# Kernel tuning notes

Measured on AMD Instinct MI355X. Metric: run time of the kernel, lower is better.

## Reference

```python
import jax, jax.numpy as jnp
import numpy as np

NB_USERS = 100000
NB_MOVIES = 20000
K = 64
N = 2000000
MAX_RATING = 5.0


def setup_inputs() -> dict:
    key = jax.random.key(0)
    ks = jax.random.split(key, 8)
    return {
        "x_users": jnp.arange(NB_USERS, dtype=jnp.int32),  # every user queried once -> original's user filter is identity
        "x_movies": jax.random.randint(ks[0], (NB_USERS,), 0, NB_MOVIES),
        "data_users": jax.random.randint(ks[1], (N,), 0, NB_USERS),
        "data_movies": jax.random.randint(ks[2], (N,), 0, NB_MOVIES),
        "data_ratings": jax.random.uniform(ks[3], (N,), dtype=jnp.float32) * MAX_RATING,
        "movies_features": jax.random.normal(ks[4], (NB_MOVIES, K), dtype=jnp.float32),
        "W_r": jax.random.normal(ks[5], (K, 1), dtype=jnp.float32) * 0.1,
        "b_r": jnp.zeros((K,), dtype=jnp.float32),
        "W_c": jax.random.normal(ks[6], (K, K), dtype=jnp.float32) * 0.1,
        "b_c": jnp.zeros((K,), dtype=jnp.float32),
        "w_out": jax.random.normal(ks[7], (1, 1), dtype=jnp.float32),
        "b_out": jnp.zeros((1,), dtype=jnp.float32),
    }


def reference(x_users, x_movies, data_users, data_movies, data_ratings,
              movies_features, W_r, b_r, W_c, b_c, w_out, b_out):
    # movies_ratings_func: Linear(1,k) + sigmoid on normalized ratings
    ratings = jax.nn.sigmoid((data_ratings[:, None] / MAX_RATING) @ W_r.T + b_r)  # [N,k]
    # combined_func: Linear(k,k) + sigmoid on (gathered movie feats * rating emb)
    rbm = jax.nn.sigmoid((movies_features[data_movies] * ratings) @ W_c.T + b_c)  # [N,k]
    # scatter-add aggregate per user
    rating_by_user = jax.ops.segment_sum(rbm, data_users, num_segments=NB_USERS)  # [U,k]
    nb_ratings = jax.ops.segment_sum(jnp.ones((N,), dtype=rbm.dtype), data_users,
                                     num_segments=NB_USERS)  # [U]
    # ignore_if_seen=True path (faithful, including rbm indexed by movie id as in original)
    rating_by_user = rating_by_user.at[x_users].add(-rbm[x_movies])
    nb_ratings = nb_ratings.at[x_users].set(jnp.maximum(jnp.float32(1.0), nb_ratings[x_users] - 1.0))
    user_features = rating_by_user[x_users] / nb_ratings[x_users][:, None]  # [B,k]
    movie_features = movies_features[x_movies]  # [B,k]
    r = (movie_features * user_features).mean(-1, keepdims=True)  # [B,1]
    r = (r @ w_out.T + b_out) * MAX_RATING  # result_func then *max_rating
    return r.reshape(-1)
```

## Files before the change

kernel.cpp:

```cpp
#include <hip/hip_runtime.h>

#define NB_USERS 100000
#define NB_MOVIES 20000
#define KDIM 64
#define NPTS 2000000
#define NTILES (NPTS / 64)
#define RQ_LEVELS 8192
#define NBUCK 391
#define CHUNK 4096
#define NCHUNK ((NPTS + CHUNK - 1) / CHUNK)
#define BCAP 6400
#define LOG2E 1.44269504088896f

typedef _Float16 f16x8 __attribute__((ext_vector_type(8)));
typedef float    f32x4 __attribute__((ext_vector_type(4)));

__device__ __forceinline__ float sigmoidf(float z) {
    return 1.0f / (1.0f + __expf(-z));
}
__device__ __forceinline__ float sigmoid_w(float w) {
    return __builtin_amdgcn_rcpf(1.0f + __builtin_amdgcn_exp2f(w));
}


__global__ __launch_bounds__(256) void mf16_kernel(
    const float* __restrict__ mf, _Float16* __restrict__ mf16)
{
    const int idx = blockIdx.x * 256 + threadIdx.x;
    if (idx < NB_MOVIES * KDIM) mf16[idx] = (_Float16)mf[idx];
}

__global__ __launch_bounds__(256) void rtab16_kernel(
    const float* __restrict__ W_r, const float* __restrict__ b_r,
    _Float16* __restrict__ rtab16)
{
    const int idx = blockIdx.x * 256 + threadIdx.x;
    const int total = (RQ_LEVELS + 1) * KDIM;
    if (idx >= total) return;
    const int q = idx >> 6, k = idx & 63;
    rtab16[idx] = (_Float16)sigmoidf(fmaf((float)q * (1.0f / RQ_LEVELS), W_r[k], b_r[k]));
}

__global__ __launch_bounds__(256) void wcfrag_kernel(
    const float* __restrict__ W_c, _Float16* __restrict__ wcfrag)
{
    const int idx = blockIdx.x * 256 + threadIdx.x;
    if (idx >= 8 * 64) return;
    const int ntkt = idx >> 6;
    const int nt = ntkt >> 1, kt = ntkt & 1;
    const int lane = idx & 63;
    const float* src = &W_c[(nt * 16 + (lane & 15)) * KDIM + kt * 32 + (lane >> 4) * 8];
    _Float16* dst = wcfrag + (size_t)ntkt * 512 + lane * 8;
    #pragma unroll
    for (int e = 0; e < 8; ++e) dst[e] = (_Float16)(src[e] * -LOG2E);
}

__global__ __launch_bounds__(256) void bucket_hist_kernel(
    const int* __restrict__ du, int* __restrict__ bhist)
{
    __shared__ int h[NBUCK];
    for (int b = threadIdx.x; b < NBUCK; b += 256) h[b] = 0;
    __syncthreads();
    int i = blockIdx.x * 256 + threadIdx.x;
    const int stride = gridDim.x * 256;
    for (; i < NPTS; i += stride) atomicAdd(&h[du[i] >> 8], 1);
    __syncthreads();
    for (int b = threadIdx.x; b < NBUCK; b += 256)
        if (h[b]) atomicAdd(&bhist[b], h[b]);
}

__global__ __launch_bounds__(256) void bscan_kernel(
    const int* __restrict__ bhist, int* __restrict__ bstart, int* __restrict__ bcursor)
{
    __shared__ int s[512];
    const int t = threadIdx.x;
    const int v0 = (t < NBUCK) ? bhist[t] : 0;
    const int v1 = (t + 256 < NBUCK) ? bhist[t + 256] : 0;
    s[t] = v0; s[t + 256] = v1;
    __syncthreads();
    for (int d = 1; d < 512; d <<= 1) {
        const int a0 = (t >= d) ? s[t - d] : 0;
        const int a1 = (t + 256 >= d) ? s[t + 256 - d] : 0;
        __syncthreads();
        s[t] += a0; s[t + 256] += a1;
        __syncthreads();
    }
    if (t < NBUCK)       { bstart[t]       = s[t] - v0;       bcursor[t]       = s[t] - v0; }
    if (t + 256 < NBUCK) { bstart[t + 256] = s[t + 256] - v1; bcursor[t + 256] = s[t + 256] - v1; }
}

__global__ __launch_bounds__(256) void binA_kernel(
    const int* __restrict__ du, const int* __restrict__ dm,
    const float* __restrict__ dr,
    int* __restrict__ bcursor, uint2* __restrict__ binned)
{
    __shared__ uint2 buf[CHUNK];
    __shared__ int cnt[NBUCK];
    __shared__ int scn[512];
    __shared__ int sbase[NBUCK];
    __shared__ int cur[NBUCK];
    __shared__ int gbase[NBUCK];

    const int t  = threadIdx.x;
    const int c0 = blockIdx.x * CHUNK;
    const int n  = min(CHUNK, NPTS - c0);

    for (int b = t; b < NBUCK; b += 256) cnt[b] = 0;
    __syncthreads();

    uint2 p[CHUNK / 256];
    #pragma unroll
    for (int j = 0; j < CHUNK / 256; ++j) {
        const int i = c0 + j * 256 + t;
        if (j * 256 + t < n) {
            const unsigned u  = (unsigned)du[i];
            const unsigned m  = (unsigned)dm[i];
            const unsigned rq = (unsigned)(int)fmaf(dr[i], (float)RQ_LEVELS / 5.0f, 0.5f);
            p[j] = make_uint2((u << 15) | m, rq);
            atomicAdd(&cnt[u >> 8], 1);
        } else {
            p[j] = make_uint2(0xFFFFFFFFu, 0u);
        }
    }
    __syncthreads();

    scn[t]       = (t < NBUCK) ? cnt[t] : 0;
    scn[t + 256] = (t + 256 < NBUCK) ? cnt[t + 256] : 0;
    __syncthreads();
    for (int d = 1; d < 512; d <<= 1) {
        const int a0 = (t >= d) ? scn[t - d] : 0;
        const int a1 = (t + 256 >= d) ? scn[t + 256 - d] : 0;
        __syncthreads();
        scn[t] += a0; scn[t + 256] += a1;
        __syncthreads();
    }
    for (int b = t; b < NBUCK; b += 256) {
        const int e = scn[b] - cnt[b];
        sbase[b] = e;
        cur[b]   = e;
        if (cnt[b] > 0) gbase[b] = atomicAdd(&bcursor[b], cnt[b]);
    }
    __syncthreads();

    #pragma unroll
    for (int j = 0; j < CHUNK / 256; ++j) {
        if (p[j].x != 0xFFFFFFFFu) {
            const int b   = p[j].x >> 23;
            const int pos = atomicAdd(&cur[b], 1);
            buf[pos] = p[j];
        }
    }
    __syncthreads();

    for (int i = t; i < n; i += 256) {
        const uint2 q = buf[i];
        const int b = q.x >> 23;
        binned[gbase[b] + (i - sbase[b])] = q;
    }
}

__global__ __launch_bounds__(256) void binB_kernel(
    const uint2* __restrict__ binned,
    const int* __restrict__ bhist, const int* __restrict__ bstart,
    uint2* __restrict__ sorted, float* __restrict__ nbrf)
{
    __shared__ uint2 buf[BCAP];
    __shared__ int cnt[256];
    __shared__ int cur[256];

    const int t  = threadIdx.x;
    const int b  = blockIdx.x;
    const int n  = bhist[b];
    const int s0 = bstart[b];

    cnt[t] = 0;
    __syncthreads();

    for (int i = t; i < n; i += 256)
        atomicAdd(&cnt[(binned[s0 + i].x >> 15) & 255], 1);
    __syncthreads();

    const int uid = (b << 8) + t;
    if (uid < NB_USERS) nbrf[uid] = (float)cnt[t];

    const int inc = cnt[t];
    cur[t] = inc;
    __syncthreads();
    for (int d = 1; d < 256; d <<= 1) {
        const int a = (t >= d) ? cur[t - d] : 0;
        __syncthreads();
        cur[t] += a;
        __syncthreads();
    }
    const int excl = cur[t] - inc;
    __syncthreads();
    cur[t] = excl;
    __syncthreads();

    for (int i = t; i < n; i += 256) {
        const uint2 q  = binned[s0 + i];
        const int  lu  = (q.x >> 15) & 255;
        const int  pos = atomicAdd(&cur[lu], 1);
        buf[pos] = q;
    }
    __syncthreads();

    for (int i = t; i < n; i += 256)
        sorted[s0 + i] = buf[i];
}

__global__ __launch_bounds__(256) void rbm_saved_kernel(
    const int* __restrict__ dm, const float* __restrict__ dr,
    const _Float16* __restrict__ mf16, const _Float16* __restrict__ rtab16,
    const _Float16* __restrict__ wcfrag, const float* __restrict__ b_c,
    float* __restrict__ rbm_saved)
{
    __shared__ _Float16 bsh[8 * 512];
    for (int i = threadIdx.x; i < 512; i += 256)
        ((f16x8*)bsh)[i] = ((const f16x8*)wcfrag)[i];
    __syncthreads();

    const int lane = threadIdx.x & 63;
    const int wave = blockIdx.x * (blockDim.x >> 6) + (threadIdx.x >> 6);
    const int NT = (NB_MOVIES + 63) / 64;
    if (wave >= NT) return;

    float wbcv[4];
    #pragma unroll
    for (int nt = 0; nt < 4; ++nt) wbcv[nt] = -LOG2E * b_c[nt * 16 + (lane & 15)];

    const int base = wave * 64;
    const int koff = (lane >> 4) * 8;

    #pragma unroll 1
    for (int mt = 0; mt < 4; ++mt) {
        const int pg = base + mt * 16 + (lane & 15);
        int   m = 0;
        float r = 0.f;
        if (pg < NB_MOVIES) { m = dm[pg]; r = dr[pg]; }
        const int rq = (int)fmaf(r, (float)RQ_LEVELS / 5.0f, 0.5f);

        const f16x8 ma = *(const f16x8*)(mf16   + (size_t)m  * KDIM + koff);
        const f16x8 mb = *(const f16x8*)(mf16   + (size_t)m  * KDIM + 32 + koff);
        const f16x8 ta = *(const f16x8*)(rtab16 + (size_t)rq * KDIM + koff);
        const f16x8 tb = *(const f16x8*)(rtab16 + (size_t)rq * KDIM + 32 + koff);
        const f16x8 a0 = ma * ta;
        const f16x8 a1 = mb * tb;

        f32x4 acc[4];
        #pragma unroll
        for (int nt = 0; nt < 4; ++nt) {
            const f16x8 b0 = *(const f16x8*)(bsh + (nt * 2 + 0) * 512 + lane * 8);
            const f16x8 b1 = *(const f16x8*)(bsh + (nt * 2 + 1) * 512 + lane * 8);
            acc[nt] = (f32x4){0.f, 0.f, 0.f, 0.f};
            acc[nt] = __builtin_amdgcn_mfma_f32_16x16x32_f16(a0, b0, acc[nt], 0, 0, 0);
            acc[nt] = __builtin_amdgcn_mfma_f32_16x16x32_f16(a1, b1, acc[nt], 0, 0, 0);
        }

        #pragma unroll
        for (int reg = 0; reg < 4; ++reg) {
            const int prow_g = base + mt * 16 + (lane >> 4) * 4 + reg;
            if (prow_g < NB_MOVIES) {
                #pragma unroll
                for (int nt = 0; nt < 4; ++nt) {
                    const float rbm = sigmoid_w(acc[nt][reg] + wbcv[nt]);
                    rbm_saved[(size_t)prow_g * KDIM + nt * 16 + (lane & 15)] = rbm;
                }
            }
        }
    }
}

__global__ __launch_bounds__(256, 4) void phase1_sorted_kernel(
    const uint2* __restrict__ sorted_ur,
    const _Float16* __restrict__ mf16,
    const _Float16* __restrict__ rtab16,
    const _Float16* __restrict__ wcfrag,
    const float* __restrict__ b_c,
    float* __restrict__ rbu)
{
    __shared__ _Float16 bsh[8 * 512];
    for (int i = threadIdx.x; i < 512; i += 256)
        ((f16x8*)bsh)[i] = ((const f16x8*)wcfrag)[i];
    __syncthreads();

    const int lane = threadIdx.x & 63;
    const int wave = blockIdx.x * (blockDim.x >> 6) + (threadIdx.x >> 6);
    const int nwav = gridDim.x * (blockDim.x >> 6);

    float wbcv[4];
    #pragma unroll
    for (int nt = 0; nt < 4; ++nt) wbcv[nt] = -LOG2E * b_c[nt * 16 + (lane & 15)];

    const int koff = (lane >> 4) * 8;
    const int g    = lane >> 4;

    for (int it = wave; it < NTILES; it += nwav) {
        const int base = it * 64;

        #pragma unroll 1
        for (int mt = 0; mt < 4; ++mt) {
            const uint2 ur = sorted_ur[base + mt * 16 + (lane & 15)];
            const unsigned u_at = ur.x >> 15;
            const int      m    = (int)(ur.x & 0x7fffu);
            const int      rq   = (int)ur.y;

            const f16x8 ma = *(const f16x8*)(mf16   + (size_t)m  * KDIM + koff);
            const f16x8 mb = *(const f16x8*)(mf16   + (size_t)m  * KDIM + 32 + koff);
            const f16x8 ta = *(const f16x8*)(rtab16 + (size_t)rq * KDIM + koff);
            const f16x8 tb = *(const f16x8*)(rtab16 + (size_t)rq * KDIM + 32 + koff);
            const f16x8 a0 = ma * ta;
            const f16x8 a1 = mb * tb;

            f32x4 acc[4];
            #pragma unroll
            for (int nt = 0; nt < 4; ++nt) {
                const f16x8 b0 = *(const f16x8*)(bsh + (nt * 2 + 0) * 512 + lane * 8);
                const f16x8 b1 = *(const f16x8*)(bsh + (nt * 2 + 1) * 512 + lane * 8);
                acc[nt] = (f32x4){0.f, 0.f, 0.f, 0.f};
                acc[nt] = __builtin_amdgcn_mfma_f32_16x16x32_f16(a0, b0, acc[nt], 0, 0, 0);
                acc[nt] = __builtin_amdgcn_mfma_f32_16x16x32_f16(a1, b1, acc[nt], 0, 0, 0);
            }

            #pragma unroll
            for (int nt = 0; nt < 4; ++nt)
                #pragma unroll
                for (int reg = 0; reg < 4; ++reg)
                    acc[nt][reg] = sigmoid_w(acc[nt][reg] + wbcv[nt]);

            const unsigned u_prev =
                (unsigned)__shfl((int)u_at, lane - 1, 64);
            const bool boundary = ((lane & 15) == 0) || (u_at != u_prev);
            unsigned long long bm = __ballot(boundary) & 0xFFFFull;

            while (bm) {
                const int s = __builtin_ctzll(bm);
                bm &= bm - 1;
                const int e = bm ? __builtin_ctzll(bm) : 16;
                const unsigned useg =
                    (unsigned)__builtin_amdgcn_readlane((int)u_at, s);

                const int lo = s - g * 4;
                const int hi = e - g * 4;
                float p0 = 0.f, p1 = 0.f, p2 = 0.f, p3 = 0.f;
                #pragma unroll
                for (int reg = 0; reg < 4; ++reg) {
                    const bool in = (reg >= lo) && (reg < hi);
                    p0 += in ? acc[0][reg] : 0.f;
                    p1 += in ? acc[1][reg] : 0.f;
                    p2 += in ? acc[2][reg] : 0.f;
                    p3 += in ? acc[3][reg] : 0.f;
                }
                p0 += __shfl_xor(p0, 16, 64); p0 += __shfl_xor(p0, 32, 64);
                p1 += __shfl_xor(p1, 16, 64); p1 += __shfl_xor(p1, 32, 64);
                p2 += __shfl_xor(p2, 16, 64); p2 += __shfl_xor(p2, 32, 64);
                p3 += __shfl_xor(p3, 16, 64); p3 += __shfl_xor(p3, 32, 64);

                const float v01 = (g & 1) ? p1 : p0;
                const float v23 = (g & 1) ? p3 : p2;
                const float val = (g & 2) ? v23 : v01;
                atomicAdd(&rbu[(size_t)useg * KDIM + lane], val);
            }
        }
    }
}

__global__ __launch_bounds__(256) void phase2_kernel(
    const int* __restrict__ x_users,
    const int* __restrict__ x_movies,
    const float* __restrict__ mf,
    const float* __restrict__ rbu,
    const float* __restrict__ nbrf,
    const float* __restrict__ rbm_saved,
    const float* __restrict__ w_out,
    const float* __restrict__ b_out,
    float* __restrict__ out)
{
    const int lane = threadIdx.x & 63;
    const int wave = blockIdx.x * (blockDim.x >> 6) + (threadIdx.x >> 6);
    if (wave >= NB_USERS) return;

    const int u  = x_users[wave];
    const int xm = x_movies[wave];

    const float nb = fmaxf(1.0f, nbrf[u] - 1.0f);
    const float uf = (rbu[(size_t)u * KDIM + lane] -
                      rbm_saved[(size_t)xm * KDIM + lane]) / nb;
    float p = mf[(size_t)xm * KDIM + lane] * uf;

    #pragma unroll
    for (int off = 32; off > 0; off >>= 1)
        p += __shfl_xor(p, off, 64);

    if (lane == 0)
        out[wave] = (p * (1.0f / 64.0f) * w_out[0] + b_out[0]) * 5.0f;
}

extern "C" void kernel_launch(void* const* d_in, const int* in_sizes, int n_in,
                              void* d_out, int out_size, void* d_ws, size_t ws_size,
                              hipStream_t stream) {
    const int*   x_users      = (const int*)  d_in[0];
    const int*   x_movies     = (const int*)  d_in[1];
    const int*   data_users   = (const int*)  d_in[2];
    const int*   data_movies  = (const int*)  d_in[3];
    const float* data_ratings = (const float*)d_in[4];
    const float* mf           = (const float*)d_in[5];
    const float* W_r          = (const float*)d_in[6];
    const float* b_r          = (const float*)d_in[7];
    const float* W_c          = (const float*)d_in[8];
    const float* b_c          = (const float*)d_in[9];
    const float* w_out        = (const float*)d_in[10];
    const float* b_out        = (const float*)d_in[11];
    float* out = (float*)d_out;

    float*     rbu       = (float*)d_ws;
    uint2*     binned    = (uint2*)d_ws;
    float*     nbrf      = rbu + (size_t)NB_USERS * KDIM;
    float*     rbm_saved = nbrf + NB_USERS;
    uint2*     sorted_ur = (uint2*)(rbm_saved + (size_t)NB_MOVIES * KDIM);
    _Float16*  mf16      = (_Float16*)(sorted_ur + NPTS);
    _Float16*  rtab16    = mf16 + (size_t)NB_MOVIES * KDIM;
    _Float16*  wcfrag    = rtab16 + (size_t)(RQ_LEVELS + 1) * KDIM;
    int*       bhist     = (int*)(wcfrag + 8 * 512);
    int*       bstart    = bhist + NBUCK;
    int*       bcursor   = bstart + NBUCK;

    hipMemsetAsync(bhist, 0, NBUCK * sizeof(int), stream);

    mf16_kernel<<<(NB_MOVIES * KDIM + 255) / 256, 256, 0, stream>>>(mf, mf16);
    rtab16_kernel<<<((RQ_LEVELS + 1) * KDIM + 255) / 256, 256, 0, stream>>>(W_r, b_r, rtab16);
    wcfrag_kernel<<<2, 256, 0, stream>>>(W_c, wcfrag);

    bucket_hist_kernel<<<1024, 256, 0, stream>>>(data_users, bhist);
    bscan_kernel<<<1, 256, 0, stream>>>(bhist, bstart, bcursor);

    binA_kernel<<<NCHUNK, 256, 0, stream>>>(
        data_users, data_movies, data_ratings, bcursor, binned);

    rbm_saved_kernel<<<79, 256, 0, stream>>>(
        data_movies, data_ratings, mf16, rtab16, wcfrag, b_c, rbm_saved);

    binB_kernel<<<NBUCK, 256, 0, stream>>>(binned, bhist, bstart, sorted_ur, nbrf);

    hipMemsetAsync(rbu, 0, (size_t)NB_USERS * KDIM * sizeof(float), stream);

    phase1_sorted_kernel<<<2048, 256, 0, stream>>>(
        sorted_ur, mf16, rtab16, wcfrag, b_c, rbu);

    phase2_kernel<<<(NB_USERS * 64 + 255) / 256, 256, 0, stream>>>(
        x_users, x_movies, mf, rbu, nbrf, rbm_saved, w_out, b_out, out);
}
```

Before: 196.1 us.

## Halve bucket width, use four-per-thread scans, vectorize phase2 with four queries per wave

Bucket width drops from 256 to 128 users, so the binning pass makes 782 buckets and binB launches more blocks, each with a smaller shared buffer. The bucket scans in bscan and binA switch to a per-thread four-element serial sum plus a 256-wide scan. phase2 now handles four queries per wave, using float4 loads and a 16-lane reduction instead of one query per 64-lane wave. An unroll-1 pragma is also dropped from the phase1 inner loop. The BCAP of 3584 per 128-user bucket has less headroom than before, which risks overflow if user distributions are skewed.

Measured after the change: 222.9 us. +13.7%, slower.

```diff
diff --git a/kernel.cpp b/kernel.cpp
--- a/kernel.cpp
+++ b/kernel.cpp
@@ -6,10 +6,11 @@
 #define NPTS 2000000
 #define NTILES (NPTS / 64)
 #define RQ_LEVELS 8192
-#define NBUCK 391
+#define UPB2 128
+#define NBUCK 782
 #define CHUNK 4096
 #define NCHUNK ((NPTS + CHUNK - 1) / CHUNK)
-#define BCAP 6400
+#define BCAP 3584
 #define LOG2E 1.44269504088896f
 
 typedef _Float16 f16x8 __attribute__((ext_vector_type(8)));
@@ -63,7 +64,7 @@
     __syncthreads();
     int i = blockIdx.x * 256 + threadIdx.x;
     const int stride = gridDim.x * 256;
-    for (; i < NPTS; i += stride) atomicAdd(&h[du[i] >> 8], 1);
+    for (; i < NPTS; i += stride) atomicAdd(&h[du[i] >> 7], 1);
     __syncthreads();
     for (int b = threadIdx.x; b < NBUCK; b += 256)
         if (h[b]) atomicAdd(&bhist[b], h[b]);
@@ -72,21 +73,31 @@
 __global__ __launch_bounds__(256) void bscan_kernel(
     const int* __restrict__ bhist, int* __restrict__ bstart, int* __restrict__ bcursor)
 {
-    __shared__ int s[512];
+    __shared__ int scn[256];
     const int t = threadIdx.x;
-    const int v0 = (t < NBUCK) ? bhist[t] : 0;
-    const int v1 = (t + 256 < NBUCK) ? bhist[t + 256] : 0;
-    s[t] = v0; s[t + 256] = v1;
-    __syncthreads();
-    for (int d = 1; d < 512; d <<= 1) {
-        const int a0 = (t >= d) ? s[t - d] : 0;
-        const int a1 = (t + 256 >= d) ? s[t + 256 - d] : 0;
-        __syncthreads();
-        s[t] += a0; s[t + 256] += a1;
-        __syncthreads();
-    }
-    if (t < NBUCK)       { bstart[t]       = s[t] - v0;       bcursor[t]       = s[t] - v0; }
-    if (t + 256 < NBUCK) { bstart[t + 256] = s[t + 256] - v1; bcursor[t + 256] = s[t + 256] - v1; }
+    int c[4];
+    int s = 0;
+    #pragma unroll
+    for (int j = 0; j < 4; ++j) {
+        const int idx = t * 4 + j;
+        c[j] = (idx < NBUCK) ? bhist[idx] : 0;
+        s += c[j];
+    }
+    scn[t] = s;
+    __syncthreads();
+    for (int d = 1; d < 256; d <<= 1) {
+        const int a = (t >= d) ? scn[t - d] : 0;
+        __syncthreads();
+        scn[t] += a;
+        __syncthreads();
+    }
+    int run = scn[t] - s;
+    #pragma unroll
+    for (int j = 0; j < 4; ++j) {
+        const int idx = t * 4 + j;
+        if (idx < NBUCK) { bstart[idx] = run; bcursor[idx] = run; }
+        run += c[j];
+    }
 }
 
 __global__ __launch_bounds__(256) void binA_kernel(
@@ -96,7 +107,7 @@
 {
     __shared__ uint2 buf[CHUNK];
     __shared__ int cnt[NBUCK];
-    __shared__ int scn[512];
+    __shared__ int scn[256];
     __shared__ int sbase[NBUCK];
     __shared__ int cur[NBUCK];
     __shared__ int gbase[NBUCK];
@@ -117,35 +128,46 @@
             const unsigned m  = (unsigned)dm[i];
             const unsigned rq = (unsigned)(int)fmaf(dr[i], (float)RQ_LEVELS / 5.0f, 0.5f);
             p[j] = make_uint2((u << 15) | m, rq);
-            atomicAdd(&cnt[u >> 8], 1);
+            atomicAdd(&cnt[u >> 7], 1);
         } else {
             p[j] = make_uint2(0xFFFFFFFFu, 0u);
         }
     }
     __syncthreads();
 
-    scn[t]       = (t < NBUCK) ? cnt[t] : 0;
-    scn[t + 256] = (t + 256 < NBUCK) ? cnt[t + 256] : 0;
-    __syncthreads();
-    for (int d = 1; d < 512; d <<= 1) {
-        const int a0 = (t >= d) ? scn[t - d] : 0;
-        const int a1 = (t + 256 >= d) ? scn[t + 256 - d] : 0;
-        __syncthreads();
-        scn[t] += a0; scn[t + 256] += a1;
-        __syncthreads();
-    }
-    for (int b = t; b < NBUCK; b += 256) {
-        const int e = scn[b] - cnt[b];
-        sbase[b] = e;
-        cur[b]   = e;
-        if (cnt[b] > 0) gbase[b] = atomicAdd(&bcursor[b], cnt[b]);
+    int c4[4];
+    int s = 0;
+    #pragma unroll
+    for (int j = 0; j < 4; ++j) {
+        const int idx = t * 4 + j;
+        c4[j] = (idx < NBUCK) ? cnt[idx] : 0;
+        s += c4[j];
+    }
+    scn[t] = s;
+    __syncthreads();
+    for (int d = 1; d < 256; d <<= 1) {
+        const int a = (t >= d) ? scn[t - d] : 0;
+        __syncthreads();
+        scn[t] += a;
+        __syncthreads();
+    }
+    int run = scn[t] - s;
+    #pragma unroll
+    for (int j = 0; j < 4; ++j) {
+        const int idx = t * 4 + j;
+        if (idx < NBUCK) {
+            sbase[idx] = run;
+            cur[idx]   = run;
+            if (c4[j] > 0) gbase[idx] = atomicAdd(&bcursor[idx], c4[j]);
+        }
+        run += c4[j];
     }
     __syncthreads();
 
     #pragma unroll
     for (int j = 0; j < CHUNK / 256; ++j) {
         if (p[j].x != 0xFFFFFFFFu) {
-            const int b   = p[j].x >> 23;
+            const int b   = p[j].x >> 22;
             const int pos = atomicAdd(&cur[b], 1);
             buf[pos] = p[j];
         }
@@ -154,7 +176,7 @@
 
     for (int i = t; i < n; i += 256) {
         const uint2 q = buf[i];
-        const int b = q.x >> 23;
+        const int b = q.x >> 22;
         binned[gbase[b] + (i - sbase[b])] = q;
     }
 }
@@ -165,41 +187,39 @@
     uint2* __restrict__ sorted, float* __restrict__ nbrf)
 {
     __shared__ uint2 buf[BCAP];
-    __shared__ int cnt[256];
-    __shared__ int cur[256];
+    __shared__ int cnt[UPB2];
+    __shared__ int cur[UPB2];
 
     const int t  = threadIdx.x;
     const int b  = blockIdx.x;
     const int n  = bhist[b];
     const int s0 = bstart[b];
 
-    cnt[t] = 0;
+    if (t < UPB2) cnt[t] = 0;
     __syncthreads();
 
     for (int i = t; i < n; i += 256)
-        atomicAdd(&cnt[(binned[s0 + i].x >> 15) & 255], 1);
-    __syncthreads();
-
-    const int uid = (b << 8) + t;
-    if (uid < NB_USERS) nbrf[uid] = (float)cnt[t];
-
-    const int inc = cnt[t];
-    cur[t] = inc;
-    __syncthreads();
-    for (int d = 1; d < 256; d <<= 1) {
-        const int a = (t >= d) ? cur[t - d] : 0;
-        __syncthreads();
-        cur[t] += a;
-        __syncthreads();
-    }
-    const int excl = cur[t] - inc;
-    __syncthreads();
-    cur[t] = excl;
+        atomicAdd(&cnt[(binned[s0 + i].x >> 15) & (UPB2 - 1)], 1);
+    __syncthreads();
+
+    const int uid = b * UPB2 + t;
+    if (t < UPB2 && uid < NB_USERS) nbrf[uid] = (float)cnt[t];
+
+    const int inc = (t < UPB2) ? cnt[t] : 0;
+    if (t < UPB2) cur[t] = inc;
+    __syncthreads();
+    for (int d = 1; d < UPB2; d <<= 1) {
+        const int a = (t < UPB2 && t >= d) ? cur[t - d] : 0;
+        __syncthreads();
+        if (t < UPB2) cur[t] += a;
+        __syncthreads();
+    }
+    if (t < UPB2) cur[t] -= inc;
     __syncthreads();
 
     for (int i = t; i < n; i += 256) {
         const uint2 q  = binned[s0 + i];
-        const int  lu  = (q.x >> 15) & 255;
+        const int  lu  = (q.x >> 15) & (UPB2 - 1);
         const int  pos = atomicAdd(&cur[lu], 1);
         buf[pos] = q;
     }
@@ -298,7 +318,6 @@
     for (int it = wave; it < NTILES; it += nwav) {
         const int base = it * 64;
 
-        #pragma unroll 1
         for (int mt = 0; mt < 4; ++mt) {
             const uint2 ur = sorted_ur[base + mt * 16 + (lane & 15)];
             const unsigned u_at = ur.x >> 15;
@@ -378,22 +397,30 @@
 {
     const int lane = threadIdx.x & 63;
     const int wave = blockIdx.x * (blockDim.x >> 6) + (threadIdx.x >> 6);
-    if (wave >= NB_USERS) return;
-
-    const int u  = x_users[wave];
-    const int xm = x_movies[wave];
-
+    const int q = wave * 4 + (lane >> 4);
+    if (q >= NB_USERS) return;
+    const int e4 = (lane & 15) * 4;
+
+    const int u  = x_users[q];
+    const int xm = x_movies[q];
     const float nb = fmaxf(1.0f, nbrf[u] - 1.0f);
-    const float uf = (rbu[(size_t)u * KDIM + lane] -
-                      rbm_saved[(size_t)xm * KDIM + lane]) / nb;
-    float p = mf[(size_t)xm * KDIM + lane] * uf;
-
-    #pragma unroll
-    for (int off = 32; off > 0; off >>= 1)
-        p += __shfl_xor(p, off, 64);
-
-    if (lane == 0)
-        out[wave] = (p * (1.0f / 64.0f) * w_out[0] + b_out[0]) * 5.0f;
+
+    const f32x4 rb = *(const f32x4*)(rbu       + (size_t)u  * KDIM + e4);
+    const f32x4 rs = *(const f32x4*)(rbm_saved + (size_t)xm * KDIM + e4);
+    const f32x4 mv = *(const f32x4*)(mf        + (size_t)xm * KDIM + e4);
+
+    float p = 0.f;
+    #pragma unroll
+    for (int e = 0; e < 4; ++e)
+        p += mv[e] * (rb[e] - rs[e]);
+
+    p += __shfl_xor(p, 1, 64);
+    p += __shfl_xor(p, 2, 64);
+    p += __shfl_xor(p, 4, 64);
+    p += __shfl_xor(p, 8, 64);
+
+    if ((lane & 15) == 0)
+        out[q] = ((p / nb) * (1.0f / 64.0f) * w_out[0] + b_out[0]) * 5.0f;
 }
 
 extern "C" void kernel_launch(void* const* d_in, const int* in_sizes, int n_in,
@@ -447,6 +474,6 @@
     phase1_sorted_kernel<<<2048, 256, 0, stream>>>(
         sorted_ur, mf16, rtab16, wcfrag, b_c, rbu);
 
-    phase2_kernel<<<(NB_USERS * 64 + 255) / 256, 256, 0, stream>>>(
+    phase2_kernel<<<(NB_USERS / 4 + 3) / 4, 256, 0, stream>>>(
         x_users, x_movies, mf, rbu, nbrf, rbm_saved, w_out, b_out, out);
 }
```
